# Kernel optimization log

Measured on AMD Instinct MI355X. Metric: run time of the kernel, lower is better.

Reference implementation:

```python
import jax, jax.numpy as jnp
import numpy as np

G, NP, K, H, DH, D, NL = 256, 1000, 8, 8, 10, 80, 10  # graphs, nodes/graph, knn, heads, d_head, hidden, layers


def setup_inputs() -> dict:
    key = jax.random.key(0)
    ks = jax.random.split(key, 16)
    rn = lambda k, shape: (jax.random.normal(k, shape, jnp.float32) * 0.05)
    return dict(
        h_feat=jax.random.normal(ks[0], (G, NP, 9), jnp.float32),
        bn_gamma=jnp.ones((9,), jnp.float32), bn_beta=jnp.zeros((9,), jnp.float32),
        W_emb=rn(ks[1], (9, D)), b_emb=jnp.zeros((D,), jnp.float32),
        Wq=rn(ks[2], (NL, D, D)), Wk=rn(ks[3], (NL, D, D)), Wv=rn(ks[4], (NL, D, D)),
        Wo=rn(ks[5], (NL, D, D)), bo=jnp.zeros((NL, D), jnp.float32),
        W1=rn(ks[6], (NL, D, 2 * D)), b1=jnp.zeros((NL, 2 * D), jnp.float32),
        W2=rn(ks[7], (NL, 2 * D, D)), b2=jnp.zeros((NL, D), jnp.float32),
        Wr0=rn(ks[8], (D, 40)), br0=jnp.zeros((40,), jnp.float32),
        Wr1=rn(ks[9], (40, 20)), br1=jnp.zeros((20,), jnp.float32),
        Wr2=rn(ks[10], (20, 64)), br2=jnp.zeros((64,), jnp.float32),
        W_clust=rn(ks[11], (64, 3)),
        W_beta=rn(ks[12], (64, 1)), b_beta=jnp.zeros((1,), jnp.float32),
    )


def _forward(h_feat, bn_gamma, bn_beta, W_emb, b_emb, Wq, Wk, Wv, Wo, bo,
             W1, b1, W2, b2, Wr0, br0, Wr1, br1, Wr2, br2, W_clust, W_beta, b_beta):
    # knn graph on raw coords (first 3 feature columns), per graph, k=8 (self included)
    coords = h_feat[..., :3]
    d2 = jnp.sum((coords[:, :, None, :] - coords[:, None, :, :]) ** 2, -1)  # [G,NP,NP]
    nbr = jax.lax.top_k(-d2, K)[1]  # [G,NP,K] neighbor indices per destination node
    gidx = jnp.arange(G)[:, None, None]

    # BatchNorm1d (training-mode batch stats over all nodes) + embedding
    x = h_feat.reshape(-1, 9)
    mu = x.mean(0)
    var = x.var(0)
    x = (x - mu) / jnp.sqrt(var + 1e-5) * bn_gamma + bn_beta
    h = (x @ W_emb + b_emb).reshape(G, NP, D)

    inv_sqrt_d = jnp.float32(1.0 / np.sqrt(DH))

    def layer(h, p):
        wq, wk, wv, wo, bo_, w1, b1_, w2, b2_ = p
        q = (h @ wq).reshape(G, NP, H, DH)
        k_ = (h @ wk).reshape(G, NP, H, DH)
        v = (h @ wv).reshape(G, NP, H, DH)
        kn = k_[gidx, nbr]  # [G,NP,K,H,DH] gather src K over edges
        vn = v[gidx, nbr]
        s = jnp.einsum('gnkhd,gnhd->gnkh', kn, q) * inv_sqrt_d
        s = jnp.exp(jnp.clip(s, -5.0, 5.0))  # scaled_exp with clamp
        wV = jnp.einsum('gnkh,gnkhd->gnhd', s, vn)
        attn = (wV / (s.sum(2)[..., None] + 1e-6)).reshape(G, NP, D)
        h = h + attn @ wo + bo_  # O proj + residual (no LN/BN)
        h = h + jax.nn.relu(h @ w1 + b1_) @ w2 + b2_  # FFN + residual
        return h, None

    h, _ = jax.lax.scan(layer, h, (Wq, Wk, Wv, Wo, bo, W1, b1, W2, b2))

    # MLPReadout 80->40->20->64 (ReLU between), then clustering coords + beta
    y = h.reshape(-1, D)
    y = jax.nn.relu(y @ Wr0 + br0)
    y = jax.nn.relu(y @ Wr1 + br1)
    y = y @ Wr2 + br2
    cc = y @ W_clust  # [N,3], no bias
    beta = y @ W_beta + b_beta  # [N,1]
    return jnp.concatenate([cc, beta], axis=1)  # [N,4]


def reference(h_feat, bn_gamma, bn_beta, W_emb, b_emb, Wq, Wk, Wv, Wo, bo,
              W1, b1, W2, b2, Wr0, br0, Wr1, br1, Wr2, br2, W_clust, W_beta, b_beta):
    return _forward(h_feat, bn_gamma, bn_beta, W_emb, b_emb, Wq, Wk, Wv, Wo, bo,
                    W1, b1, W2, b2, Wr0, br0, Wr1, br1, Wr2, br2, W_clust, W_beta, b_beta)
```

## Files before the change

### kernel.cpp

```cpp
#include <hip/hip_runtime.h>
#include <cstdint>
#include <cstddef>


typedef __attribute__((ext_vector_type(8))) short short8v;
typedef __attribute__((ext_vector_type(4))) float f32x4;

#define MFMA16(ACC, A, B) ACC = __builtin_amdgcn_mfma_f32_16x16x32_bf16(A, B, ACC, 0, 0, 0)
#define MF3(ACC, AH, AL, BH, BL) { MFMA16(ACC, AH, BH); MFMA16(ACC, AH, BL); MFMA16(ACC, AL, BH); }

__device__ __forceinline__ void splitbf(float x, unsigned short& hi, unsigned short& lo) {
  unsigned u = __float_as_uint(x);
  unsigned r = u + 0x7FFFu + ((u >> 16) & 1u);
  hi = (unsigned short)(r >> 16);
  float hf = __uint_as_float(((unsigned)hi) << 16);
  float lf = x - hf;
  unsigned u2 = __float_as_uint(lf);
  unsigned r2 = u2 + 0x7FFFu + ((u2 >> 16) & 1u);
  lo = (unsigned short)(r2 >> 16);
}

__device__ __forceinline__ float bf2f(unsigned short v) {
  return __uint_as_float(((unsigned)v) << 16);
}
// ... 89 lines not shown
      ss[f] += __shfl_down(ss[f], off);
    }
  }
  int wid = threadIdx.x >> 6, lane = threadIdx.x & 63;
  if (lane == 0) {
    #pragma unroll
    for (int f = 0; f < 9; ++f) { red[wid][f] = s[f]; red[wid][9 + f] = ss[f]; }
  }
  __syncthreads();
  if (threadIdx.x < 18) {
    partial[(size_t)blockIdx.x * 18 + threadIdx.x] =
        red[0][threadIdx.x] + red[1][threadIdx.x] + red[2][threadIdx.x] + red[3][threadIdx.x];
  }
}

__global__ __launch_bounds__(256) void bn_stat2(const float* __restrict__ partial, float* __restrict__ stats) {
  __shared__ double sd[9][28], qd[9][28];
  int tid = threadIdx.x;
  if (tid < 252) {
    int f = tid % 9, gq = tid / 9;
    double s = 0.0, q = 0.0;
    for (int b = gq; b < 1000; b += 28) {
      s += (double)partial[b * 18 + f];
      q += (double)partial[b * 18 + 9 + f];
    }
    sd[f][gq] = s;
    qd[f][gq] = q;
  }
  __syncthreads();
  if (tid < 9) {
    double s = 0.0, q = 0.0;
    for (int g2 = 0; g2 < 28; ++g2) { s += sd[tid][g2]; q += qd[tid][g2]; }
    double mu = s / 256000.0;
    double var = q / 256000.0 - mu * mu;
    stats[tid] = (float)mu;
    stats[9 + tid] = (float)(1.0 / sqrt(var + 1e-5));
  }
}

__global__ __launch_bounds__(256) void split_tr(const float* __restrict__ src, unsigned short* __restrict__ dhi,
                                                unsigned short* __restrict__ dlo, int R, int C, int KS) {
  const float* s = src + (size_t)blockIdx.x * R * C;
  unsigned short* dh = dhi + (size_t)blockIdx.x * C * KS;
  unsigned short* dl = dlo + (size_t)blockIdx.x * C * KS;
  int n = C * KS;
  for (int i = threadIdx.x; i < n; i += 256) {
    int c = i / KS, kk = i % KS;
    float v = (kk < R) ? s[kk * C + c] : 0.f;
    unsigned short h, l;
    splitbf(v, h, l);
    dh[i] = h;
    dl[i] = l;
  }
}

__global__ __launch_bounds__(320) void embed_kernel(const float* __restrict__ hf, const float* __restrict__ stats,
                                                    const float* __restrict__ gamma, const float* __restrict__ beta,
                                                    const float* __restrict__ We, const float* __restrict__ be,
                                                    float* __restrict__ h) {
  __shared__ __align__(16) float xs[40 * 9];
  size_t p0 = (size_t)blockIdx.x * 40;
  for (int i = threadIdx.x; i < 360; i += 320) {
    int f = i % 9;
    float x = hf[p0 * 9 + i];
    xs[i] = (x - stats[f]) * stats[9 + f] * gamma[f] + beta[f];
  }
  __syncthreads();
  int c = threadIdx.x % 80, pg = threadIdx.x / 80;
  float we[9];
  #pragma unroll
  for (int f = 0; f < 9; ++f) we[f] = We[f * 80 + c];
  float bias = be[c];
  for (int pp = 0; pp < 10; ++pp) {
    int p = pg * 10 + pp;
    float acc = 0.f;
    #pragma unroll
    for (int f = 0; f < 9; ++f) acc = fmaf(xs[p * 9 + f], we[f], acc);
    h[(p0 + p) * 80 + c] = acc + bias;
  }
}

__global__ __launch_bounds__(320) void kv_kernel(const float* __restrict__ h,
                                                 const unsigned short* __restrict__ WkH, const unsigned short* __restrict__ WkL,
                                                 const unsigned short* __restrict__ WvH, const unsigned short* __restrict__ WvL,
                                                 float* __restrict__ kb, float* __restrict__ vb) {
  __shared__ __align__(16) unsigned short ahi[48 * 104];
  __shared__ __align__(16) unsigned short alo[48 * 104];
  int b = blockIdx.x;
  int xcd = b & 7;
  int r = b >> 3;
  int graph = (xcd << 5) + (r / 25);
  int jb = r % 25;
  size_t p0 = (size_t)graph * 1000 + (size_t)jb * 40;
  int tid = threadIdx.x;
  int lane = tid & 63, wv = tid >> 6;
  int fr = lane & 15, fq = lane >> 4;
  for (int i = tid; i < 800; i += 320) {
    int row = i / 20, kq = i % 20;
    float4 v = reinterpret_cast<const float4*>(h + (p0 + row) * 80)[kq];
    unsigned short h0, l0, h1, l1, h2, l2, h3, l3;
    splitbf(v.x, h0, l0); splitbf(v.y, h1, l1); splitbf(v.z, h2, l2); splitbf(v.w, h3, l3);
    int off = row * 104 + kq * 4;
    *reinterpret_cast<unsigned*>(&ahi[off]) = (unsigned)h0 | ((unsigned)h1 << 16);
    *reinterpret_cast<unsigned*>(&ahi[off + 2]) = (unsigned)h2 | ((unsigned)h3 << 16);
    *reinterpret_cast<unsigned*>(&alo[off]) = (unsigned)l0 | ((unsigned)l1 << 16);
    *reinterpret_cast<unsigned*>(&alo[off + 2]) = (unsigned)l2 | ((unsigned)l3 << 16);
  }
  for (int i = tid; i < 384; i += 320) {
    int row = i >> 3, kk = 80 + ((i & 7) << 1);
    int off = row * 104 + kk;
    *reinterpret_cast<unsigned*>(&ahi[off]) = 0u;
    *reinterpret_cast<unsigned*>(&alo[off]) = 0u;
  }
  __syncthreads();
  int bcol = wv * 16 + fr;
  f32x4 ck0 = {0.f, 0.f, 0.f, 0.f}, ck1 = ck0, ck2 = ck0;
  f32x4 cv0 = ck0, cv1 = ck0, cv2 = ck0;
  #pragma unroll
  for (int ks = 0; ks < 3; ++ks) {
    int boff = bcol * 96 + ks * 32 + fq * 8;
    short8v bkh = *reinterpret_cast<const short8v*>(WkH + boff);
    short8v bkl = *reinterpret_cast<const short8v*>(WkL + boff);
    short8v bvh = *reinterpret_cast<const short8v*>(WvH + boff);
    short8v bvl = *reinterpret_cast<const short8v*>(WvL + boff);
    int a0 = (0 * 16 + fr) * 104 + ks * 32 + fq * 8;
    int a1 = (1 * 16 + fr) * 104 + ks * 32 + fq * 8;
    int a2 = (2 * 16 + fr) * 104 + ks * 32 + fq * 8;
    short8v ah0 = *reinterpret_cast<const short8v*>(ahi + a0);
    short8v al0 = *reinterpret_cast<const short8v*>(alo + a0);
    MF3(ck0, ah0, al0, bkh, bkl); MF3(cv0, ah0, al0, bvh, bvl);
    short8v ah1 = *reinterpret_cast<const short8v*>(ahi + a1);
    short8v al1 = *reinterpret_cast<const short8v*>(alo + a1);
    MF3(ck1, ah1, al1, bkh, bkl); MF3(cv1, ah1, al1, bvh, bvl);
    short8v ah2 = *reinterpret_cast<const short8v*>(ahi + a2);
    short8v al2 = *reinterpret_cast<const short8v*>(alo + a2);
    MF3(ck2, ah2, al2, bkh, bkl); MF3(cv2, ah2, al2, bvh, bvl);
  }
  #pragma unroll
  for (int j = 0; j < 4; ++j) {
    int r0 = fq * 4 + j;
    kb[(p0 + r0) * 80 + bcol] = ck0[j];
    vb[(p0 + r0) * 80 + bcol] = cv0[j];
    int r1 = 16 + r0;
    kb[(p0 + r1) * 80 + bcol] = ck1[j];
    vb[(p0 + r1) * 80 + bcol] = cv1[j];
    int r2 = 32 + r0;
    if (r2 < 40) {
      kb[(p0 + r2) * 80 + bcol] = ck2[j];
      vb[(p0 + r2) * 80 + bcol] = cv2[j];
    }
  }
}

__global__ __launch_bounds__(320) void battn_kernel(const float* __restrict__ h, const float* __restrict__ kb,
                                                    const float* __restrict__ vb, const int* __restrict__ nbr,
                                                    const unsigned short* __restrict__ WqH, const unsigned short* __restrict__ WqL,
                                                    const unsigned short* __restrict__ WoH, const unsigned short* __restrict__ WoL,
                                                    const float* __restrict__ bo,
                                                    const unsigned short* __restrict__ W1H, const unsigned short* __restrict__ W1L,
                                                    const float* __restrict__ b1,
                                                    const unsigned short* __restrict__ W2H, const unsigned short* __restrict__ W2L,
                                                    const float* __restrict__ b2, float* __restrict__ hout) {
  __shared__ __align__(16) unsigned short ahi[48 * 168];
  __shared__ __align__(16) unsigned short alo[48 * 168];
  int b = blockIdx.x;
  int xcd = b & 7;
  int r = b >> 3;
  int graph = (xcd << 5) + (r / 25);
  int jb = r % 25;
  size_t gbase = (size_t)graph * 1000;
  size_t pbase = gbase + (size_t)jb * 40;
  int tid = threadIdx.x;
  int lane = tid & 63, wv = tid >> 6;
  int fr = lane & 15, fq = lane >> 4;
  int bcol = wv * 16 + fr;
  int pA = tid >> 3, hhA = tid & 7;
  int nb[8];
  #pragma unroll
  for (int kk = 0; kk < 8; ++kk) nb[kk] = nbr[(pbase + pA) * 8 + kk];
  float hres0[4], hres1[4], hres2[4];
  #pragma unroll
  for (int j = 0; j < 4; ++j) {
    int r0 = fq * 4 + j;
    hres0[j] = h[(pbase + r0) * 80 + bcol];
    hres1[j] = h[(pbase + 16 + r0) * 80 + bcol];
    int r2 = 32 + r0;
    hres2[j] = (r2 < 40) ? h[(pbase + r2) * 80 + bcol] : 0.f;
  }
  for (int i = tid; i < 800; i += 320) {
    int row = i / 20, kq = i % 20;
    float4 v = reinterpret_cast<const float4*>(h + (pbase + row) * 80)[kq];
    unsigned short h0, l0, h1, l1, h2_, l2, h3, l3;
    splitbf(v.x, h0, l0); splitbf(v.y, h1, l1); splitbf(v.z, h2_, l2); splitbf(v.w, h3, l3);
    int off = row * 168 + kq * 4;
    *reinterpret_cast<unsigned*>(&ahi[off]) = (unsigned)h0 | ((unsigned)h1 << 16);
    *reinterpret_cast<unsigned*>(&ahi[off + 2]) = (unsigned)h2_ | ((unsigned)h3 << 16);
    *reinterpret_cast<unsigned*>(&alo[off]) = (unsigned)l0 | ((unsigned)l1 << 16);
    *reinterpret_cast<unsigned*>(&alo[off + 2]) = (unsigned)l2 | ((unsigned)l3 << 16);
  }
  for (int i = tid; i < 384; i += 320) {
    int row = i >> 3, kk = 80 + ((i & 7) << 1);
    int off = row * 168 + kk;
    *reinterpret_cast<unsigned*>(&ahi[off]) = 0u;
    *reinterpret_cast<unsigned*>(&alo[off]) = 0u;
  }
  __syncthreads();
  f32x4 q0 = {0.f, 0.f, 0.f, 0.f}, q1 = q0, q2 = q0;
  {
    #pragma unroll
    for (int ks = 0; ks < 3; ++ks) {
      int boff = bcol * 96 + ks * 32 + fq * 8;
      short8v bh = *reinterpret_cast<const short8v*>(WqH + boff);
      short8v bl = *reinterpret_cast<const short8v*>(WqL + boff);
      int a0 = (0 * 16 + fr) * 168 + ks * 32 + fq * 8;
      int a1 = (1 * 16 + fr) * 168 + ks * 32 + fq * 8;
      int a2 = (2 * 16 + fr) * 168 + ks * 32 + fq * 8;
      short8v ah0 = *reinterpret_cast<const short8v*>(ahi + a0);
      short8v al0 = *reinterpret_cast<const short8v*>(alo + a0);
      MF3(q0, ah0, al0, bh, bl);
      short8v ah1 = *reinterpret_cast<const short8v*>(ahi + a1);
      short8v al1 = *reinterpret_cast<const short8v*>(alo + a1);
      MF3(q1, ah1, al1, bh, bl);
      short8v ah2 = *reinterpret_cast<const short8v*>(ahi + a2);
      short8v al2 = *reinterpret_cast<const short8v*>(alo + a2);
      MF3(q2, ah2, al2, bh, bl);
    }
  }
  __syncthreads();
  {
    #pragma unroll
    for (int j = 0; j < 4; ++j) {
      unsigned short hh_, ll_;
      int r0 = fq * 4 + j;
      splitbf(q0[j], hh_, ll_);
      ahi[r0 * 168 + bcol] = hh_; alo[r0 * 168 + bcol] = ll_;
      int r1 = 16 + r0;
      splitbf(q1[j], hh_, ll_);
      ahi[r1 * 168 + bcol] = hh_; alo[r1 * 168 + bcol] = ll_;
      int r2 = 32 + r0;
      if (r2 < 40) {
        splitbf(q2[j], hh_, ll_);
        ahi[r2 * 168 + bcol] = hh_; alo[r2 * 168 + bcol] = ll_;
      }
    }
  }
  __syncthreads();
  {
    int p = pA, hh = hhA;
    float qv[10];
    #pragma unroll
    for (int d2 = 0; d2 < 5; ++d2) {
      int off = p * 168 + hh * 10 + 2 * d2;
      unsigned uh = *reinterpret_cast<const unsigned*>(&ahi[off]);
      unsigned ul = *reinterpret_cast<const unsigned*>(&alo[off]);
      qv[2 * d2] = bf2f((unsigned short)uh) + bf2f((unsigned short)ul);
      qv[2 * d2 + 1] = bf2f((unsigned short)(uh >> 16)) + bf2f((unsigned short)(ul >> 16));
    }
    float sv[8];
    float denom = 0.f;
    #pragma unroll
    for (int kk = 0; kk < 8; ++kk) {
      const float2* kr = reinterpret_cast<const float2*>(kb + (gbase + nb[kk]) * 80 + hh * 10);
      float acc = 0.f;
      #pragma unroll
      for (int d2 = 0; d2 < 5; ++d2) {
        float2 kv2 = kr[d2];
        acc = fmaf(qv[2 * d2], kv2.x, acc);
        acc = fmaf(qv[2 * d2 + 1], kv2.y, acc);
      }
      float s = acc * 0.31622776601683794f;
      s = fminf(fmaxf(s, -5.f), 5.f);
      s = expf(s);
      sv[kk] = s;
      denom += s;
    }
    float wV[10] = {0, 0, 0, 0, 0, 0, 0, 0, 0, 0};
    #pragma unroll
    for (int kk = 0; kk < 8; ++kk) {
      const float2* vr = reinterpret_cast<const float2*>(vb + (gbase + nb[kk]) * 80 + hh * 10);
      #pragma unroll
      for (int d2 = 0; d2 < 5; ++d2) {
        float2 vv = vr[d2];
        wV[2 * d2] = fmaf(sv[kk], vv.x, wV[2 * d2]);
        wV[2 * d2 + 1] = fmaf(sv[kk], vv.y, wV[2 * d2 + 1]);
      }
    }
    float dn = denom + 1e-6f;
    #pragma unroll
    for (int d2 = 0; d2 < 5; ++d2) {
      float x0 = wV[2 * d2] / dn;
      float x1 = wV[2 * d2 + 1] / dn;
      unsigned short h0, l0, h1, l1;
      splitbf(x0, h0, l0); splitbf(x1, h1, l1);
      int off = p * 168 + hh * 10 + 2 * d2;
      *reinterpret_cast<unsigned*>(&ahi[off]) = (unsigned)h0 | ((unsigned)h1 << 16);
      *reinterpret_cast<unsigned*>(&alo[off]) = (unsigned)l0 | ((unsigned)l1 << 16);
    }
  }
  __syncthreads();
  f32x4 o0 = {0.f, 0.f, 0.f, 0.f}, o1 = o0, o2 = o0;
  {
    #pragma unroll
    for (int ks = 0; ks < 3; ++ks) {
      int boff = bcol * 96 + ks * 32 + fq * 8;
      short8v bh = *reinterpret_cast<const short8v*>(WoH + boff);
      short8v bl = *reinterpret_cast<const short8v*>(WoL + boff);
      int a0 = (0 * 16 + fr) * 168 + ks * 32 + fq * 8;
      int a1 = (1 * 16 + fr) * 168 + ks * 32 + fq * 8;
      int a2 = (2 * 16 + fr) * 168 + ks * 32 + fq * 8;
      short8v ah0 = *reinterpret_cast<const short8v*>(ahi + a0);
      short8v al0 = *reinterpret_cast<const short8v*>(alo + a0);
      MF3(o0, ah0, al0, bh, bl);
      short8v ah1 = *reinterpret_cast<const short8v*>(ahi + a1);
      short8v al1 = *reinterpret_cast<const short8v*>(alo + a1);
      MF3(o1, ah1, al1, bh, bl);
      short8v ah2 = *reinterpret_cast<const short8v*>(ahi + a2);
      short8v al2 = *reinterpret_cast<const short8v*>(alo + a2);
      MF3(o2, ah2, al2, bh, bl);
    }
  }
  __syncthreads();
  {
    float bias = bo[bcol];
    #pragma unroll
    for (int j = 0; j < 4; ++j) {
      unsigned short hh_, ll_;
      int r0 = fq * 4 + j;
      o0[j] = hres0[j] + o0[j] + bias;
      splitbf(o0[j], hh_, ll_);
      ahi[r0 * 168 + bcol] = hh_; alo[r0 * 168 + bcol] = ll_;
      int r1 = 16 + r0;
      o1[j] = hres1[j] + o1[j] + bias;
      splitbf(o1[j], hh_, ll_);
      ahi[r1 * 168 + bcol] = hh_; alo[r1 * 168 + bcol] = ll_;
      int r2 = 32 + r0;
      if (r2 < 40) {
        o2[j] = hres2[j] + o2[j] + bias;
        splitbf(o2[j], hh_, ll_);
        ahi[r2 * 168 + bcol] = hh_; alo[r2 * 168 + bcol] = ll_;
      }
    }
  }
  __syncthreads();
  f32x4 t00 = {0.f, 0.f, 0.f, 0.f}, t01 = t00, t02 = t00;
  f32x4 t10 = t00, t11 = t00, t12 = t00;
  {
    int bc0 = wv * 16 + fr, bc1 = (wv + 5) * 16 + fr;
    #pragma unroll
    for (int ks = 0; ks < 3; ++ks) {
      int b0 = bc0 * 96 + ks * 32 + fq * 8;
      int b1o = bc1 * 96 + ks * 32 + fq * 8;
      short8v bh0 = *reinterpret_cast<const short8v*>(W1H + b0);
      short8v bl0 = *reinterpret_cast<const short8v*>(W1L + b0);
      short8v bh1 = *reinterpret_cast<const short8v*>(W1H + b1o);
      short8v bl1 = *reinterpret_cast<const short8v*>(W1L + b1o);
      int a0 = (0 * 16 + fr) * 168 + ks * 32 + fq * 8;
      int a1 = (1 * 16 + fr) * 168 + ks * 32 + fq * 8;
      int a2 = (2 * 16 + fr) * 168 + ks * 32 + fq * 8;
      short8v ah0 = *reinterpret_cast<const short8v*>(ahi + a0);
      short8v al0 = *reinterpret_cast<const short8v*>(alo + a0);
      MF3(t00, ah0, al0, bh0, bl0); MF3(t10, ah0, al0, bh1, bl1);
      short8v ah1 = *reinterpret_cast<const short8v*>(ahi + a1);
      short8v al1 = *reinterpret_cast<const short8v*>(alo + a1);
      MF3(t01, ah1, al1, bh0, bl0); MF3(t11, ah1, al1, bh1, bl1);
      short8v ah2 = *reinterpret_cast<const short8v*>(ahi + a2);
      short8v al2 = *reinterpret_cast<const short8v*>(alo + a2);
      MF3(t02, ah2, al2, bh0, bl0); MF3(t12, ah2, al2, bh1, bl1);
    }
  }
  __syncthreads();
  {
    int bc0 = wv * 16 + fr, bc1 = (wv + 5) * 16 + fr;
    float bias0 = b1[bc0], bias1 = b1[bc1];
    #pragma unroll
    for (int j = 0; j < 4; ++j) {
      unsigned short hh_, ll_;
      int r0 = fq * 4 + j;
      float t = fmaxf(t00[j] + bias0, 0.f);
      splitbf(t, hh_, ll_); ahi[r0 * 168 + bc0] = hh_; alo[r0 * 168 + bc0] = ll_;
      t = fmaxf(t10[j] + bias1, 0.f);
      splitbf(t, hh_, ll_); ahi[r0 * 168 + bc1] = hh_; alo[r0 * 168 + bc1] = ll_;
      int r1 = 16 + r0;
      t = fmaxf(t01[j] + bias0, 0.f);
      splitbf(t, hh_, ll_); ahi[r1 * 168 + bc0] = hh_; alo[r1 * 168 + bc0] = ll_;
      t = fmaxf(t11[j] + bias1, 0.f);
      splitbf(t, hh_, ll_); ahi[r1 * 168 + bc1] = hh_; alo[r1 * 168 + bc1] = ll_;
      int r2 = 32 + r0;
      if (r2 < 40) {
        t = fmaxf(t02[j] + bias0, 0.f);
        splitbf(t, hh_, ll_); ahi[r2 * 168 + bc0] = hh_; alo[r2 * 168 + bc0] = ll_;
        t = fmaxf(t12[j] + bias1, 0.f);
        splitbf(t, hh_, ll_); ahi[r2 * 168 + bc1] = hh_; alo[r2 * 168 + bc1] = ll_;
      }
    }
  }
  __syncthreads();
  {
    f32x4 c0 = {0.f, 0.f, 0.f, 0.f}, c1 = c0, c2 = c0;
    #pragma unroll
    for (int ks = 0; ks < 5; ++ks) {
      int boff = bcol * 160 + ks * 32 + fq * 8;
      short8v bh = *reinterpret_cast<const short8v*>(W2H + boff);
      short8v bl = *reinterpret_cast<const short8v*>(W2L + boff);
      int a0 = (0 * 16 + fr) * 168 + ks * 32 + fq * 8;
      int a1 = (1 * 16 + fr) * 168 + ks * 32 + fq * 8;
      int a2 = (2 * 16 + fr) * 168 + ks * 32 + fq * 8;
      short8v ah0 = *reinterpret_cast<const short8v*>(ahi + a0);
      short8v al0 = *reinterpret_cast<const short8v*>(alo + a0);
      MF3(c0, ah0, al0, bh, bl);
      short8v ah1 = *reinterpret_cast<const short8v*>(ahi + a1);
      short8v al1 = *reinterpret_cast<const short8v*>(alo + a1);
      MF3(c1, ah1, al1, bh, bl);
      short8v ah2 = *reinterpret_cast<const short8v*>(ahi + a2);
      short8v al2 = *reinterpret_cast<const short8v*>(alo + a2);
      MF3(c2, ah2, al2, bh, bl);
    }
    float bias = b2[bcol];
    #pragma unroll
    for (int j = 0; j < 4; ++j) {
      int r0 = fq * 4 + j;
      hout[(pbase + r0) * 80 + bcol] = o0[j] + c0[j] + bias;
      int r1 = 16 + r0;
      hout[(pbase + r1) * 80 + bcol] = o1[j] + c1[j] + bias;
      int r2 = 32 + r0;
      if (r2 < 40) hout[(pbase + r2) * 80 + bcol] = o2[j] + c2[j] + bias;
    }
  }
}

__global__ __launch_bounds__(320) void readout_kernel(const float* __restrict__ h, const float* __restrict__ Wr0,
                                                      const float* __restrict__ br0, const float* __restrict__ Wr1,
                                                      const float* __restrict__ br1, const float* __restrict__ Wr2,
                                                      const float* __restrict__ br2, const float* __restrict__ Wc,
                                                      const float* __restrict__ Wb, const float* __restrict__ bb,
                                                      float* __restrict__ out) {
  __shared__ __align__(16) float hs[3200];
  __shared__ __align__(16) float y0s[40 * 40];
  __shared__ __align__(16) float y1s[40 * 20];
  __shared__ __align__(16) float y2s[40 * 64];
  size_t p0 = (size_t)blockIdx.x * 40;
  int tid = threadIdx.x;
  {
    const float4* src = reinterpret_cast<const float4*>(h + p0 * 80);
    float4* dst = reinterpret_cast<float4*>(hs);
    for (int i = tid; i < 800; i += 320) dst[i] = src[i];
  }
  __syncthreads();
  {
    int c = tid % 40, grp = tid / 40;
    if (grp < 5) {
      float wcol[80];
      #pragma unroll
      for (int kk = 0; kk < 80; ++kk) wcol[kk] = Wr0[kk * 40 + c];
      float bias = br0[c];
      float acc[8] = {};
      #pragma unroll
      for (int j = 0; j < 8; ++j) {
        const float4* r4 = reinterpret_cast<const float4*>(hs + (grp * 8 + j) * 80);
        #pragma unroll
        for (int kq = 0; kq < 20; ++kq) {
          float4 hv = r4[kq];
          acc[j] = fmaf(hv.x, wcol[4 * kq + 0], acc[j]);
          acc[j] = fmaf(hv.y, wcol[4 * kq + 1], acc[j]);
          acc[j] = fmaf(hv.z, wcol[4 * kq + 2], acc[j]);
          acc[j] = fmaf(hv.w, wcol[4 * kq + 3], acc[j]);
        }
      }
      #pragma unroll
      for (int j = 0; j < 8; ++j) y0s[(grp * 8 + j) * 40 + c] = fmaxf(acc[j] + bias, 0.f);
    }
  }
  __syncthreads();
  {
    int c = tid % 20, grp = tid / 20;
    if (grp < 5) {
      float wcol[40];
      #pragma unroll
      for (int kk = 0; kk < 40; ++kk) wcol[kk] = Wr1[kk * 20 + c];
      float bias = br1[c];
      float acc[8] = {};
      #pragma unroll
      for (int j = 0; j < 8; ++j) {
        const float4* r4 = reinterpret_cast<const float4*>(y0s + (grp * 8 + j) * 40);
        #pragma unroll
        for (int kq = 0; kq < 10; ++kq) {
          float4 hv = r4[kq];
          acc[j] = fmaf(hv.x, wcol[4 * kq + 0], acc[j]);
          acc[j] = fmaf(hv.y, wcol[4 * kq + 1], acc[j]);
          acc[j] = fmaf(hv.z, wcol[4 * kq + 2], acc[j]);
          acc[j] = fmaf(hv.w, wcol[4 * kq + 3], acc[j]);
        }
      }
      #pragma unroll
      for (int j = 0; j < 8; ++j) y1s[(grp * 8 + j) * 20 + c] = fmaxf(acc[j] + bias, 0.f);
    }
  }
  __syncthreads();
  {
    int c = tid % 64, grp = tid / 64;
    float wcol[20];
    #pragma unroll
    for (int kk = 0; kk < 20; ++kk) wcol[kk] = Wr2[kk * 64 + c];
    float bias = br2[c];
    float acc[8] = {};
    #pragma unroll
    for (int j = 0; j < 8; ++j) {
      const float4* r4 = reinterpret_cast<const float4*>(y1s + (grp * 8 + j) * 20);
      #pragma unroll
      for (int kq = 0; kq < 5; ++kq) {
        float4 hv = r4[kq];
        acc[j] = fmaf(hv.x, wcol[4 * kq + 0], acc[j]);
        acc[j] = fmaf(hv.y, wcol[4 * kq + 1], acc[j]);
        acc[j] = fmaf(hv.z, wcol[4 * kq + 2], acc[j]);
        acc[j] = fmaf(hv.w, wcol[4 * kq + 3], acc[j]);
      }
    }
    #pragma unroll
    for (int j = 0; j < 8; ++j) y2s[(grp * 8 + j) * 64 + c] = acc[j] + bias;
  }
  __syncthreads();
  {
    int c = tid % 4, p = tid / 4;
    if (p < 40) {
      float wcol[64];
      if (c < 3) {
        #pragma unroll
        for (int kk = 0; kk < 64; ++kk) wcol[kk] = Wc[kk * 3 + c];
      } else {
        #pragma unroll
        for (int kk = 0; kk < 64; ++kk) wcol[kk] = Wb[kk];
      }
      float acc = 0.f;
      #pragma unroll
      for (int kk = 0; kk < 64; ++kk) acc = fmaf(y2s[p * 64 + kk], wcol[kk], acc);
      if (c == 3) acc += bb[0];
      out[(p0 + p) * 4 + c] = acc;
    }
  }
}

extern "C" void kernel_launch(void* const* d_in, const int* in_sizes, int n_in,
                              void* d_out, int out_size, void* d_ws, size_t ws_size,
                              hipStream_t stream) {
  const float* hf = (const float*)d_in[0];
  const float* gamma = (const float*)d_in[1];
  const float* beta = (const float*)d_in[2];
  const float* We = (const float*)d_in[3];
  const float* be = (const float*)d_in[4];
  const float* Wq = (const float*)d_in[5];
  const float* Wk = (const float*)d_in[6];
  const float* Wv = (const float*)d_in[7];
  const float* Wo = (const float*)d_in[8];
  const float* bo = (const float*)d_in[9];
  const float* W1 = (const float*)d_in[10];
  const float* b1 = (const float*)d_in[11];
  const float* W2 = (const float*)d_in[12];
  const float* b2 = (const float*)d_in[13];
  const float* Wr0 = (const float*)d_in[14];
  const float* br0 = (const float*)d_in[15];
  const float* Wr1 = (const float*)d_in[16];
  const float* br1 = (const float*)d_in[17];
  const float* Wr2 = (const float*)d_in[18];
  const float* br2 = (const float*)d_in[19];
  const float* Wc = (const float*)d_in[20];
  const float* Wb = (const float*)d_in[21];
  const float* bb = (const float*)d_in[22];
  float* out = (float*)d_out;

  char* wsp = (char*)d_ws;
  int* nbr = (int*)wsp;            wsp += (size_t)256000 * 8 * 4;
  float* hA = (float*)wsp;         wsp += (size_t)256000 * 80 * 4;
  float* kbuf = (float*)wsp;       wsp += (size_t)256000 * 80 * 4;
  float* vbuf = (float*)wsp;       wsp += (size_t)256000 * 80 * 4;
  float* partial = (float*)wsp;    wsp += (size_t)1000 * 18 * 4;
  float* stats = (float*)wsp;      wsp += 128;
  unsigned short* WqH = (unsigned short*)wsp; wsp += (size_t)10 * 7680 * 2;
  unsigned short* WqL = (unsigned short*)wsp; wsp += (size_t)10 * 7680 * 2;
  unsigned short* WkH = (unsigned short*)wsp; wsp += (size_t)10 * 7680 * 2;
  unsigned short* WkL = (unsigned short*)wsp; wsp += (size_t)10 * 7680 * 2;
  unsigned short* WvH = (unsigned short*)wsp; wsp += (size_t)10 * 7680 * 2;
  unsigned short* WvL = (unsigned short*)wsp; wsp += (size_t)10 * 7680 * 2;
  unsigned short* WoH = (unsigned short*)wsp; wsp += (size_t)10 * 7680 * 2;
  unsigned short* WoL = (unsigned short*)wsp; wsp += (size_t)10 * 7680 * 2;
  unsigned short* W1H = (unsigned short*)wsp; wsp += (size_t)10 * 15360 * 2;
  unsigned short* W1L = (unsigned short*)wsp; wsp += (size_t)10 * 15360 * 2;
  unsigned short* W2H = (unsigned short*)wsp; wsp += (size_t)10 * 12800 * 2;
  unsigned short* W2L = (unsigned short*)wsp; wsp += (size_t)10 * 12800 * 2;

  knn_kernel<<<1024, 256, 0, stream>>>(hf, nbr);
  bn_stat1<<<1000, 256, 0, stream>>>(hf, partial);
  bn_stat2<<<1, 256, 0, stream>>>(partial, stats);
  split_tr<<<10, 256, 0, stream>>>(Wq, WqH, WqL, 80, 80, 96);
  split_tr<<<10, 256, 0, stream>>>(Wk, WkH, WkL, 80, 80, 96);
  split_tr<<<10, 256, 0, stream>>>(Wv, WvH, WvL, 80, 80, 96);
  split_tr<<<10, 256, 0, stream>>>(Wo, WoH, WoL, 80, 80, 96);
  split_tr<<<10, 256, 0, stream>>>(W1, W1H, W1L, 80, 160, 96);
  split_tr<<<10, 256, 0, stream>>>(W2, W2H, W2L, 160, 80, 160);
  embed_kernel<<<6400, 320, 0, stream>>>(hf, stats, gamma, beta, We, be, hA);
  for (int l = 0; l < 10; ++l) {
    kv_kernel<<<6400, 320, 0, stream>>>(hA, WkH + (size_t)l * 7680, WkL + (size_t)l * 7680,
                                        WvH + (size_t)l * 7680, WvL + (size_t)l * 7680, kbuf, vbuf);
    battn_kernel<<<6400, 320, 0, stream>>>(hA, kbuf, vbuf, nbr,
                                           WqH + (size_t)l * 7680, WqL + (size_t)l * 7680,
                                           WoH + (size_t)l * 7680, WoL + (size_t)l * 7680, bo + (size_t)l * 80,
                                           W1H + (size_t)l * 15360, W1L + (size_t)l * 15360, b1 + (size_t)l * 160,
                                           W2H + (size_t)l * 12800, W2L + (size_t)l * 12800, b2 + (size_t)l * 80, hA);
  }
  readout_kernel<<<6400, 320, 0, stream>>>(hA, Wr0, br0, Wr1, br1, Wr2, br2, Wc, Wb, bb, out);
}
```

Baseline: 3.429 ms.

## Enlarge battn row tile from 40 to 80 nodes per block

The fused attention/FFN kernel now handles 80 rows per block instead of 40, so each block uses 5 full 16-row MFMA tiles instead of 3 with padding. Each thread runs the gather-attention for two points, and the grid shrinks to 13 tiles per graph, the last one half-filled. The aim is to amortise weight fragment loads and the padding waste across more rows. In exchange, LDS use per block roughly doubles and register pressure rises, which may lower occupancy, and the last tile in each graph wastes compute on zero-padded rows.

```diff
diff --git a/kernel.cpp b/kernel.cpp
--- a/kernel.cpp
+++ b/kernel.cpp
@@ -265,6 +265,60 @@
   }
 }
 
+__device__ __forceinline__ void attn_point(int p, int hh, const int* __restrict__ nb, size_t gbase,
+                                           const float* __restrict__ kb, const float* __restrict__ vb,
+                                           unsigned short* __restrict__ ahi, unsigned short* __restrict__ alo) {
+  float qv[10];
+  #pragma unroll
+  for (int d2 = 0; d2 < 5; ++d2) {
+    int off = p * 168 + hh * 10 + 2 * d2;
+    unsigned uh = *reinterpret_cast<const unsigned*>(&ahi[off]);
+    unsigned ul = *reinterpret_cast<const unsigned*>(&alo[off]);
+    qv[2 * d2] = bf2f((unsigned short)uh) + bf2f((unsigned short)ul);
+    qv[2 * d2 + 1] = bf2f((unsigned short)(uh >> 16)) + bf2f((unsigned short)(ul >> 16));
+  }
+  float sv[8];
+  float denom = 0.f;
+  #pragma unroll
+  for (int kk = 0; kk < 8; ++kk) {
+    const float2* kr = reinterpret_cast<const float2*>(kb + (gbase + nb[kk]) * 80 + hh * 10);
+    float acc = 0.f;
+    #pragma unroll
+    for (int d2 = 0; d2 < 5; ++d2) {
+      float2 kv2 = kr[d2];
+      acc = fmaf(qv[2 * d2], kv2.x, acc);
+      acc = fmaf(qv[2 * d2 + 1], kv2.y, acc);
+    }
+    float s = acc * 0.31622776601683794f;
+    s = fminf(fmaxf(s, -5.f), 5.f);
+    s = expf(s);
+    sv[kk] = s;
+    denom += s;
+  }
+  float wV[10] = {0, 0, 0, 0, 0, 0, 0, 0, 0, 0};
+  #pragma unroll
+  for (int kk = 0; kk < 8; ++kk) {
+    const float2* vr = reinterpret_cast<const float2*>(vb + (gbase + nb[kk]) * 80 + hh * 10);
+    #pragma unroll
+    for (int d2 = 0; d2 < 5; ++d2) {
+      float2 vv = vr[d2];
+      wV[2 * d2] = fmaf(sv[kk], vv.x, wV[2 * d2]);
+      wV[2 * d2 + 1] = fmaf(sv[kk], vv.y, wV[2 * d2 + 1]);
+    }
+  }
+  float dn = denom + 1e-6f;
+  #pragma unroll
+  for (int d2 = 0; d2 < 5; ++d2) {
+    float x0 = wV[2 * d2] / dn;
+    float x1 = wV[2 * d2 + 1] / dn;
+    unsigned short h0, l0, h1, l1;
+    splitbf(x0, h0, l0); splitbf(x1, h1, l1);
+    int off = p * 168 + hh * 10 + 2 * d2;
+    *reinterpret_cast<unsigned*>(&ahi[off]) = (unsigned)h0 | ((unsigned)h1 << 16);
+    *reinterpret_cast<unsigned*>(&alo[off]) = (unsigned)l0 | ((unsigned)l1 << 16);
+  }
+}
+
 __global__ __launch_bounds__(320) void battn_kernel(const float* __restrict__ h, const float* __restrict__ kb,
                                                     const float* __restrict__ vb, const int* __restrict__ nbr,
                                                     const unsigned short* __restrict__ WqH, const unsigned short* __restrict__ WqL,
@@ -274,35 +328,43 @@
                                                     const float* __restrict__ b1,
                                                     const unsigned short* __restrict__ W2H, const unsigned short* __restrict__ W2L,
                                                     const float* __restrict__ b2, float* __restrict__ hout) {
-  __shared__ __align__(16) unsigned short ahi[48 * 168];
-  __shared__ __align__(16) unsigned short alo[48 * 168];
+  __shared__ __align__(16) unsigned short ahi[80 * 168];
+  __shared__ __align__(16) unsigned short alo[80 * 168];
   int b = blockIdx.x;
   int xcd = b & 7;
   int r = b >> 3;
-  int graph = (xcd << 5) + (r / 25);
-  int jb = r % 25;
+  int graph = (xcd << 5) + (r / 13);
+  int t13 = r % 13;
   size_t gbase = (size_t)graph * 1000;
-  size_t pbase = gbase + (size_t)jb * 40;
+  size_t pbase = gbase + (size_t)t13 * 80;
+  int nrows = (t13 == 12) ? 40 : 80;
   int tid = threadIdx.x;
   int lane = tid & 63, wv = tid >> 6;
   int fr = lane & 15, fq = lane >> 4;
   int bcol = wv * 16 + fr;
-  int pA = tid >> 3, hhA = tid & 7;
-  int nb[8];
-  #pragma unroll
-  for (int kk = 0; kk < 8; ++kk) nb[kk] = nbr[(pbase + pA) * 8 + kk];
-  float hres0[4], hres1[4], hres2[4];
-  #pragma unroll
-  for (int j = 0; j < 4; ++j) {
-    int r0 = fq * 4 + j;
-    hres0[j] = h[(pbase + r0) * 80 + bcol];
-    hres1[j] = h[(pbase + 16 + r0) * 80 + bcol];
-    int r2 = 32 + r0;
-    hres2[j] = (r2 < 40) ? h[(pbase + r2) * 80 + bcol] : 0.f;
-  }
-  for (int i = tid; i < 800; i += 320) {
+  int p1 = tid >> 3, hhA = tid & 7;
+  int p2 = p1 + 40;
+  bool has2 = p2 < nrows;
+  int nb1[8], nb2[8];
+  #pragma unroll
+  for (int kk = 0; kk < 8; ++kk) nb1[kk] = nbr[(pbase + p1) * 8 + kk];
+  if (has2) {
+    #pragma unroll
+    for (int kk = 0; kk < 8; ++kk) nb2[kk] = nbr[(pbase + p2) * 8 + kk];
+  }
+  float hres[5][4];
+  #pragma unroll
+  for (int t = 0; t < 5; ++t) {
+    #pragma unroll
+    for (int j = 0; j < 4; ++j) {
+      int row = t * 16 + fq * 4 + j;
+      hres[t][j] = (row < nrows) ? h[(pbase + row) * 80 + bcol] : 0.f;
+    }
+  }
+  for (int i = tid; i < 1600; i += 320) {
     int row = i / 20, kq = i % 20;
-    float4 v = reinterpret_cast<const float4*>(h + (pbase + row) * 80)[kq];
+    float4 v = {0.f, 0.f, 0.f, 0.f};
+    if (row < nrows) v = reinterpret_cast<const float4*>(h + (pbase + row) * 80)[kq];
     unsigned short h0, l0, h1, l1, h2_, l2, h3, l3;
     splitbf(v.x, h0, l0); splitbf(v.y, h1, l1); splitbf(v.z, h2_, l2); splitbf(v.w, h3, l3);
     int off = row * 168 + kq * 4;
@@ -311,32 +373,37 @@
     *reinterpret_cast<unsigned*>(&alo[off]) = (unsigned)l0 | ((unsigned)l1 << 16);
     *reinterpret_cast<unsigned*>(&alo[off + 2]) = (unsigned)l2 | ((unsigned)l3 << 16);
   }
-  for (int i = tid; i < 384; i += 320) {
+  for (int i = tid; i < 640; i += 320) {
     int row = i >> 3, kk = 80 + ((i & 7) << 1);
     int off = row * 168 + kk;
     *reinterpret_cast<unsigned*>(&ahi[off]) = 0u;
     *reinterpret_cast<unsigned*>(&alo[off]) = 0u;
   }
   __syncthreads();
-  f32x4 q0 = {0.f, 0.f, 0.f, 0.f}, q1 = q0, q2 = q0;
+  f32x4 q0 = {0.f, 0.f, 0.f, 0.f}, q1 = q0, q2 = q0, q3 = q0, q4 = q0;
   {
     #pragma unroll
     for (int ks = 0; ks < 3; ++ks) {
       int boff = bcol * 96 + ks * 32 + fq * 8;
       short8v bh = *reinterpret_cast<const short8v*>(WqH + boff);
       short8v bl = *reinterpret_cast<const short8v*>(WqL + boff);
-      int a0 = (0 * 16 + fr) * 168 + ks * 32 + fq * 8;
-      int a1 = (1 * 16 + fr) * 168 + ks * 32 + fq * 8;
-      int a2 = (2 * 16 + fr) * 168 + ks * 32 + fq * 8;
-      short8v ah0 = *reinterpret_cast<const short8v*>(ahi + a0);
-      short8v al0 = *reinterpret_cast<const short8v*>(alo + a0);
-      MF3(q0, ah0, al0, bh, bl);
-      short8v ah1 = *reinterpret_cast<const short8v*>(ahi + a1);
-      short8v al1 = *reinterpret_cast<const short8v*>(alo + a1);
-      MF3(q1, ah1, al1, bh, bl);
-      short8v ah2 = *reinterpret_cast<const short8v*>(ahi + a2);
-      short8v al2 = *reinterpret_cast<const short8v*>(alo + a2);
-      MF3(q2, ah2, al2, bh, bl);
+      int ab = fr * 168 + ks * 32 + fq * 8;
+      short8v ah, al;
+      ah = *reinterpret_cast<const short8v*>(ahi + ab);
+      al = *reinterpret_cast<const short8v*>(alo + ab);
+      MF3(q0, ah, al, bh, bl);
+      ah = *reinterpret_cast<const short8v*>(ahi + ab + 16 * 168);
+      al = *reinterpret_cast<const short8v*>(alo + ab + 16 * 168);
+      MF3(q1, ah, al, bh, bl);
+      ah = *reinterpret_cast<const short8v*>(ahi + ab + 32 * 168);
+      al = *reinterpret_cast<const short8v*>(alo + ab + 32 * 168);
+      MF3(q2, ah, al, bh, bl);
+      ah = *reinterpret_cast<const short8v*>(ahi + ab + 48 * 168);
+      al = *reinterpret_cast<const short8v*>(alo + ab + 48 * 168);
+      MF3(q3, ah, al, bh, bl);
+      ah = *reinterpret_cast<const short8v*>(ahi + ab + 64 * 168);
+      al = *reinterpret_cast<const short8v*>(alo + ab + 64 * 168);
+      MF3(q4, ah, al, bh, bl);
     }
   }
   __syncthreads();
@@ -344,92 +411,42 @@
     #pragma unroll
     for (int j = 0; j < 4; ++j) {
       unsigned short hh_, ll_;
-      int r0 = fq * 4 + j;
-      splitbf(q0[j], hh_, ll_);
-      ahi[r0 * 168 + bcol] = hh_; alo[r0 * 168 + bcol] = ll_;
-      int r1 = 16 + r0;
-      splitbf(q1[j], hh_, ll_);
-      ahi[r1 * 168 + bcol] = hh_; alo[r1 * 168 + bcol] = ll_;
-      int r2 = 32 + r0;
-      if (r2 < 40) {
-        splitbf(q2[j], hh_, ll_);
-        ahi[r2 * 168 + bcol] = hh_; alo[r2 * 168 + bcol] = ll_;
-      }
-    }
-  }
-  __syncthreads();
-  {
-    int p = pA, hh = hhA;
-    float qv[10];
-    #pragma unroll
-    for (int d2 = 0; d2 < 5; ++d2) {
-      int off = p * 168 + hh * 10 + 2 * d2;
-      unsigned uh = *reinterpret_cast<const unsigned*>(&ahi[off]);
-      unsigned ul = *reinterpret_cast<const unsigned*>(&alo[off]);
-      qv[2 * d2] = bf2f((unsigned short)uh) + bf2f((unsigned short)ul);
-      qv[2 * d2 + 1] = bf2f((unsigned short)(uh >> 16)) + bf2f((unsigned short)(ul >> 16));
-    }
-    float sv[8];
-    float denom = 0.f;
-    #pragma unroll
-    for (int kk = 0; kk < 8; ++kk) {
-      const float2* kr = reinterpret_cast<const float2*>(kb + (gbase + nb[kk]) * 80 + hh * 10);
-      float acc = 0.f;
-      #pragma unroll
-      for (int d2 = 0; d2 < 5; ++d2) {
-        float2 kv2 = kr[d2];
-        acc = fmaf(qv[2 * d2], kv2.x, acc);
-        acc = fmaf(qv[2 * d2 + 1], kv2.y, acc);
-      }
-      float s = acc * 0.31622776601683794f;
-      s = fminf(fmaxf(s, -5.f), 5.f);
-      s = expf(s);
-      sv[kk] = s;
-      denom += s;
-    }
-    float wV[10] = {0, 0, 0, 0, 0, 0, 0, 0, 0, 0};
-    #pragma unroll
-    for (int kk = 0; kk < 8; ++kk) {
-      const float2* vr = reinterpret_cast<const float2*>(vb + (gbase + nb[kk]) * 80 + hh * 10);
-      #pragma unroll
-      for (int d2 = 0; d2 < 5; ++d2) {
-        float2 vv = vr[d2];
-        wV[2 * d2] = fmaf(sv[kk], vv.x, wV[2 * d2]);
-        wV[2 * d2 + 1] = fmaf(sv[kk], vv.y, wV[2 * d2 + 1]);
-      }
-    }
-    float dn = denom + 1e-6f;
-    #pragma unroll
-    for (int d2 = 0; d2 < 5; ++d2) {
-      float x0 = wV[2 * d2] / dn;
-      float x1 = wV[2 * d2 + 1] / dn;
-      unsigned short h0, l0, h1, l1;
-      splitbf(x0, h0, l0); splitbf(x1, h1, l1);
-      int off = p * 168 + hh * 10 + 2 * d2;
-      *reinterpret_cast<unsigned*>(&ahi[off]) = (unsigned)h0 | ((unsigned)h1 << 16);
-      *reinterpret_cast<unsigned*>(&alo[off]) = (unsigned)l0 | ((unsigned)l1 << 16);
-    }
-  }
-  __syncthreads();
-  f32x4 o0 = {0.f, 0.f, 0.f, 0.f}, o1 = o0, o2 = o0;
+      int rb = fq * 4 + j;
+      splitbf(q0[j], hh_, ll_); ahi[rb * 168 + bcol] = hh_; alo[rb * 168 + bcol] = ll_;
+      splitbf(q1[j], hh_, ll_); ahi[(16 + rb) * 168 + bcol] = hh_; alo[(16 + rb) * 168 + bcol] = ll_;
+      splitbf(q2[j], hh_, ll_); ahi[(32 + rb) * 168 + bcol] = hh_; alo[(32 + rb) * 168 + bcol] = ll_;
+      splitbf(q3[j], hh_, ll_); ahi[(48 + rb) * 168 + bcol] = hh_; alo[(48 + rb) * 168 + bcol] = ll_;
+      splitbf(q4[j], hh_, ll_); ahi[(64 + rb) * 168 + bcol] = hh_; alo[(64 + rb) * 168 + bcol] = ll_;
+    }
+  }
+  __syncthreads();
+  attn_point(p1, hhA, nb1, gbase, kb, vb, ahi, alo);
+  if (has2) attn_point(p2, hhA, nb2, gbase, kb, vb, ahi, alo);
+  __syncthreads();
+  f32x4 o0 = {0.f, 0.f, 0.f, 0.f}, o1 = o0, o2 = o0, o3 = o0, o4 = o0;
   {
     #pragma unroll
     for (int ks = 0; ks < 3; ++ks) {
       int boff = bcol * 96 + ks * 32 + fq * 8;
       short8v bh = *reinterpret_cast<const short8v*>(WoH + boff);
       short8v bl = *reinterpret_cast<const short8v*>(WoL + boff);
-      int a0 = (0 * 16 + fr) * 168 + ks * 32 + fq * 8;
-      int a1 = (1 * 16 + fr) * 168 + ks * 32 + fq * 8;
-      int a2 = (2 * 16 + fr) * 168 + ks * 32 + fq * 8;
-      short8v ah0 = *reinterpret_cast<const short8v*>(ahi + a0);
-      short8v al0 = *reinterpret_cast<const short8v*>(alo + a0);
-      MF3(o0, ah0, al0, bh, bl);
-      short8v ah1 = *reinterpret_cast<const short8v*>(ahi + a1);
-      short8v al1 = *reinterpret_cast<const short8v*>(alo + a1);
-      MF3(o1, ah1, al1, bh, bl);
-      short8v ah2 = *reinterpret_cast<const short8v*>(ahi + a2);
-      short8v al2 = *reinterpret_cast<const short8v*>(alo + a2);
-      MF3(o2, ah2, al2, bh, bl);
+      int ab = fr * 168 + ks * 32 + fq * 8;
+      short8v ah, al;
+      ah = *reinterpret_cast<const short8v*>(ahi + ab);
+      al = *reinterpret_cast<const short8v*>(alo + ab);
+      MF3(o0, ah, al, bh, bl);
+      ah = *reinterpret_cast<const short8v*>(ahi + ab + 16 * 168);
+      al = *reinterpret_cast<const short8v*>(alo + ab + 16 * 168);
+      MF3(o1, ah, al, bh, bl);
+      ah = *reinterpret_cast<const short8v*>(ahi + ab + 32 * 168);
+      al = *reinterpret_cast<const short8v*>(alo + ab + 32 * 168);
+      MF3(o2, ah, al, bh, bl);
+      ah = *reinterpret_cast<const short8v*>(ahi + ab + 48 * 168);
+      al = *reinterpret_cast<const short8v*>(alo + ab + 48 * 168);
+      MF3(o3, ah, al, bh, bl);
+      ah = *reinterpret_cast<const short8v*>(ahi + ab + 64 * 168);
+      al = *reinterpret_cast<const short8v*>(alo + ab + 64 * 168);
+      MF3(o4, ah, al, bh, bl);
     }
   }
   __syncthreads();
@@ -438,25 +455,22 @@
     #pragma unroll
     for (int j = 0; j < 4; ++j) {
       unsigned short hh_, ll_;
-      int r0 = fq * 4 + j;
-      o0[j] = hres0[j] + o0[j] + bias;
-      splitbf(o0[j], hh_, ll_);
-      ahi[r0 * 168 + bcol] = hh_; alo[r0 * 168 + bcol] = ll_;
-      int r1 = 16 + r0;
-      o1[j] = hres1[j] + o1[j] + bias;
-      splitbf(o1[j], hh_, ll_);
-      ahi[r1 * 168 + bcol] = hh_; alo[r1 * 168 + bcol] = ll_;
-      int r2 = 32 + r0;
-      if (r2 < 40) {
-        o2[j] = hres2[j] + o2[j] + bias;
-        splitbf(o2[j], hh_, ll_);
-        ahi[r2 * 168 + bcol] = hh_; alo[r2 * 168 + bcol] = ll_;
-      }
-    }
-  }
-  __syncthreads();
-  f32x4 t00 = {0.f, 0.f, 0.f, 0.f}, t01 = t00, t02 = t00;
-  f32x4 t10 = t00, t11 = t00, t12 = t00;
+      int rb = fq * 4 + j;
+      o0[j] = hres[0][j] + o0[j] + bias;
+      splitbf(o0[j], hh_, ll_); ahi[rb * 168 + bcol] = hh_; alo[rb * 168 + bcol] = ll_;
+      o1[j] = hres[1][j] + o1[j] + bias;
+      splitbf(o1[j], hh_, ll_); ahi[(16 + rb) * 168 + bcol] = hh_; alo[(16 + rb) * 168 + bcol] = ll_;
+      o2[j] = hres[2][j] + o2[j] + bias;
+      splitbf(o2[j], hh_, ll_); ahi[(32 + rb) * 168 + bcol] = hh_; alo[(32 + rb) * 168 + bcol] = ll_;
+      o3[j] = hres[3][j] + o3[j] + bias;
+      splitbf(o3[j], hh_, ll_); ahi[(48 + rb) * 168 + bcol] = hh_; alo[(48 + rb) * 168 + bcol] = ll_;
+      o4[j] = hres[4][j] + o4[j] + bias;
+      splitbf(o4[j], hh_, ll_); ahi[(64 + rb) * 168 + bcol] = hh_; alo[(64 + rb) * 168 + bcol] = ll_;
+    }
+  }
+  __syncthreads();
+  f32x4 tA0 = {0.f, 0.f, 0.f, 0.f}, tA1 = tA0, tA2 = tA0, tA3 = tA0, tA4 = tA0;
+  f32x4 tB0 = tA0, tB1 = tA0, tB2 = tA0, tB3 = tA0, tB4 = tA0;
   {
     int bc0 = wv * 16 + fr, bc1 = (wv + 5) * 16 + fr;
     #pragma unroll
@@ -467,18 +481,23 @@
       short8v bl0 = *reinterpret_cast<const short8v*>(W1L + b0);
       short8v bh1 = *reinterpret_cast<const short8v*>(W1H + b1o);
       short8v bl1 = *reinterpret_cast<const short8v*>(W1L + b1o);
-      int a0 = (0 * 16 + fr) * 168 + ks * 32 + fq * 8;
-      int a1 = (1 * 16 + fr) * 168 + ks * 32 + fq * 8;
-      int a2 = (2 * 16 + fr) * 168 + ks * 32 + fq * 8;
-      short8v ah0 = *reinterpret_cast<const short8v*>(ahi + a0);
-      short8v al0 = *reinterpret_cast<const short8v*>(alo + a0);
-      MF3(t00, ah0, al0, bh0, bl0); MF3(t10, ah0, al0, bh1, bl1);
-      short8v ah1 = *reinterpret_cast<const short8v*>(ahi + a1);
-      short8v al1 = *reinterpret_cast<const short8v*>(alo + a1);
-      MF3(t01, ah1, al1, bh0, bl0); MF3(t11, ah1, al1, bh1, bl1);
-      short8v ah2 = *reinterpret_cast<const short8v*>(ahi + a2);
-      short8v al2 = *reinterpret_cast<const short8v*>(alo + a2);
-      MF3(t02, ah2, al2, bh0, bl0); MF3(t12, ah2, al2, bh1, bl1);
+      int ab = fr * 168 + ks * 32 + fq * 8;
+      short8v ah, al;
+      ah = *reinterpret_cast<const short8v*>(ahi + ab);
+      al = *reinterpret_cast<const short8v*>(alo + ab);
+      MF3(tA0, ah, al, bh0, bl0); MF3(tB0, ah, al, bh1, bl1);
+      ah = *reinterpret_cast<const short8v*>(ahi + ab + 16 * 168);
+      al = *reinterpret_cast<const short8v*>(alo + ab + 16 * 168);
+      MF3(tA1, ah, al, bh0, bl0); MF3(tB1, ah, al, bh1, bl1);
+      ah = *reinterpret_cast<const short8v*>(ahi + ab + 32 * 168);
+      al = *reinterpret_cast<const short8v*>(alo + ab + 32 * 168);
+      MF3(tA2, ah, al, bh0, bl0); MF3(tB2, ah, al, bh1, bl1);
+      ah = *reinterpret_cast<const short8v*>(ahi + ab + 48 * 168);
+      al = *reinterpret_cast<const short8v*>(alo + ab + 48 * 168);
+      MF3(tA3, ah, al, bh0, bl0); MF3(tB3, ah, al, bh1, bl1);
+      ah = *reinterpret_cast<const short8v*>(ahi + ab + 64 * 168);
+      al = *reinterpret_cast<const short8v*>(alo + ab + 64 * 168);
+      MF3(tA4, ah, al, bh0, bl0); MF3(tB4, ah, al, bh1, bl1);
     }
   }
   __syncthreads();
@@ -488,55 +507,69 @@
     #pragma unroll
     for (int j = 0; j < 4; ++j) {
       unsigned short hh_, ll_;
-      int r0 = fq * 4 + j;
-      float t = fmaxf(t00[j] + bias0, 0.f);
-      splitbf(t, hh_, ll_); ahi[r0 * 168 + bc0] = hh_; alo[r0 * 168 + bc0] = ll_;
-      t = fmaxf(t10[j] + bias1, 0.f);
-      splitbf(t, hh_, ll_); ahi[r0 * 168 + bc1] = hh_; alo[r0 * 168 + bc1] = ll_;
-      int r1 = 16 + r0;
-      t = fmaxf(t01[j] + bias0, 0.f);
-      splitbf(t, hh_, ll_); ahi[r1 * 168 + bc0] = hh_; alo[r1 * 168 + bc0] = ll_;
-      t = fmaxf(t11[j] + bias1, 0.f);
-      splitbf(t, hh_, ll_); ahi[r1 * 168 + bc1] = hh_; alo[r1 * 168 + bc1] = ll_;
-      int r2 = 32 + r0;
-      if (r2 < 40) {
-        t = fmaxf(t02[j] + bias0, 0.f);
-        splitbf(t, hh_, ll_); ahi[r2 * 168 + bc0] = hh_; alo[r2 * 168 + bc0] = ll_;
-        t = fmaxf(t12[j] + bias1, 0.f);
-        splitbf(t, hh_, ll_); ahi[r2 * 168 + bc1] = hh_; alo[r2 * 168 + bc1] = ll_;
-      }
-    }
-  }
-  __syncthreads();
-  {
-    f32x4 c0 = {0.f, 0.f, 0.f, 0.f}, c1 = c0, c2 = c0;
+      int rb = fq * 4 + j;
+      float t;
+      t = fmaxf(tA0[j] + bias0, 0.f);
+      splitbf(t, hh_, ll_); ahi[rb * 168 + bc0] = hh_; alo[rb * 168 + bc0] = ll_;
+      t = fmaxf(tB0[j] + bias1, 0.f);
+      splitbf(t, hh_, ll_); ahi[rb * 168 + bc1] = hh_; alo[rb * 168 + bc1] = ll_;
+      t = fmaxf(tA1[j] + bias0, 0.f);
+      splitbf(t, hh_, ll_); ahi[(16 + rb) * 168 + bc0] = hh_; alo[(16 + rb) * 168 + bc0] = ll_;
+      t = fmaxf(tB1[j] + bias1, 0.f);
+      splitbf(t, hh_, ll_); ahi[(16 + rb) * 168 + bc1] = hh_; alo[(16 + rb) * 168 + bc1] = ll_;
+      t = fmaxf(tA2[j] + bias0, 0.f);
+      splitbf(t, hh_, ll_); ahi[(32 + rb) * 168 + bc0] = hh_; alo[(32 + rb) * 168 + bc0] = ll_;
+      t = fmaxf(tB2[j] + bias1, 0.f);
+      splitbf(t, hh_, ll_); ahi[(32 + rb) * 168 + bc1] = hh_; alo[(32 + rb) * 168 + bc1] = ll_;
+      t = fmaxf(tA3[j] + bias0, 0.f);
+      splitbf(t, hh_, ll_); ahi[(48 + rb) * 168 + bc0] = hh_; alo[(48 + rb) * 168 + bc0] = ll_;
+      t = fmaxf(tB3[j] + bias1, 0.f);
+      splitbf(t, hh_, ll_); ahi[(48 + rb) * 168 + bc1] = hh_; alo[(48 + rb) * 168 + bc1] = ll_;
+      t = fmaxf(tA4[j] + bias0, 0.f);
+      splitbf(t, hh_, ll_); ahi[(64 + rb) * 168 + bc0] = hh_; alo[(64 + rb) * 168 + bc0] = ll_;
+      t = fmaxf(tB4[j] + bias1, 0.f);
+      splitbf(t, hh_, ll_); ahi[(64 + rb) * 168 + bc1] = hh_; alo[(64 + rb) * 168 + bc1] = ll_;
+    }
+  }
+  __syncthreads();
+  {
+    f32x4 c0 = {0.f, 0.f, 0.f, 0.f}, c1 = c0, c2 = c0, c3 = c0, c4 = c0;
     #pragma unroll
     for (int ks = 0; ks < 5; ++ks) {
       int boff = bcol * 160 + ks * 32 + fq * 8;
       short8v bh = *reinterpret_cast<const short8v*>(W2H + boff);
       short8v bl = *reinterpret_cast<const short8v*>(W2L + boff);
-      int a0 = (0 * 16 + fr) * 168 + ks * 32 + fq * 8;
-      int a1 = (1 * 16 + fr) * 168 + ks * 32 + fq * 8;
-      int a2 = (2 * 16 + fr) * 168 + ks * 32 + fq * 8;
-      short8v ah0 = *reinterpret_cast<const short8v*>(ahi + a0);
-      short8v al0 = *reinterpret_cast<const short8v*>(alo + a0);
-      MF3(c0, ah0, al0, bh, bl);
-      short8v ah1 = *reinterpret_cast<const short8v*>(ahi + a1);
-      short8v al1 = *reinterpret_cast<const short8v*>(alo + a1);
-      MF3(c1, ah1, al1, bh, bl);
-      short8v ah2 = *reinterpret_cast<const short8v*>(ahi + a2);
-      short8v al2 = *reinterpret_cast<const short8v*>(alo + a2);
-      MF3(c2, ah2, al2, bh, bl);
+      int ab = fr * 168 + ks * 32 + fq * 8;
+      short8v ah, al;
+      ah = *reinterpret_cast<const short8v*>(ahi + ab);
+      al = *reinterpret_cast<const short8v*>(alo + ab);
+      MF3(c0, ah, al, bh, bl);
+      ah = *reinterpret_cast<const short8v*>(ahi + ab + 16 * 168);
+      al = *reinterpret_cast<const short8v*>(alo + ab + 16 * 168);
+      MF3(c1, ah, al, bh, bl);
+      ah = *reinterpret_cast<const short8v*>(ahi + ab + 32 * 168);
+      al = *reinterpret_cast<const short8v*>(alo + ab + 32 * 168);
+      MF3(c2, ah, al, bh, bl);
+      ah = *reinterpret_cast<const short8v*>(ahi + ab + 48 * 168);
+      al = *reinterpret_cast<const short8v*>(alo + ab + 48 * 168);
+      MF3(c3, ah, al, bh, bl);
+      ah = *reinterpret_cast<const short8v*>(ahi + ab + 64 * 168);
+      al = *reinterpret_cast<const short8v*>(alo + ab + 64 * 168);
+      MF3(c4, ah, al, bh, bl);
     }
     float bias = b2[bcol];
     #pragma unroll
     for (int j = 0; j < 4; ++j) {
-      int r0 = fq * 4 + j;
-      hout[(pbase + r0) * 80 + bcol] = o0[j] + c0[j] + bias;
-      int r1 = 16 + r0;
-      hout[(pbase + r1) * 80 + bcol] = o1[j] + c1[j] + bias;
-      int r2 = 32 + r0;
-      if (r2 < 40) hout[(pbase + r2) * 80 + bcol] = o2[j] + c2[j] + bias;
+      int rb = fq * 4 + j;
+      if (rb < nrows) hout[(pbase + rb) * 80 + bcol] = o0[j] + c0[j] + bias;
+      int r1 = 16 + rb;
+      if (r1 < nrows) hout[(pbase + r1) * 80 + bcol] = o1[j] + c1[j] + bias;
+      int r2 = 32 + rb;
+      if (r2 < nrows) hout[(pbase + r2) * 80 + bcol] = o2[j] + c2[j] + bias;
+      int r3 = 48 + rb;
+      if (r3 < nrows) hout[(pbase + r3) * 80 + bcol] = o3[j] + c3[j] + bias;
+      int r4 = 64 + rb;
+      if (r4 < nrows) hout[(pbase + r4) * 80 + bcol] = o4[j] + c4[j] + bias;
     }
   }
 }
@@ -713,7 +746,7 @@
   for (int l = 0; l < 10; ++l) {
     kv_kernel<<<6400, 320, 0, stream>>>(hA, WkH + (size_t)l * 7680, WkL + (size_t)l * 7680,
                                         WvH + (size_t)l * 7680, WvL + (size_t)l * 7680, kbuf, vbuf);
-    battn_kernel<<<6400, 320, 0, stream>>>(hA, kbuf, vbuf, nbr,
+    battn_kernel<<<3328, 320, 0, stream>>>(hA, kbuf, vbuf, nbr,
                                            WqH + (size_t)l * 7680, WqL + (size_t)l * 7680,
                                            WoH + (size_t)l * 7680, WoL + (size_t)l * 7680, bo + (size_t)l * 80,
                                            W1H + (size_t)l * 15360, W1L + (size_t)l * 15360, b1 + (size_t)l * 160,
```

Result: slower. 3.911 ms (+14.0%).
